# Optimization experiments

Measured on AMD Instinct MI355X. Metric: run time of the kernel, lower is better.

Reference implementation:

```python
import jax, jax.numpy as jnp
import numpy as np

B, N, F = 8, 2048, 256

def setup_inputs() -> dict:
    key = jax.random.key(0)
    ks = jax.random.split(key, 8)
    X = jax.random.normal(ks[0], (B, N, F), dtype=jnp.float32)
    A_geo = jax.random.uniform(ks[1], (N, N), dtype=jnp.float32)
    distance_matrix = jax.random.uniform(ks[2], (N, N), dtype=jnp.float32)
    W_w = jax.random.normal(ks[3], (F, F), dtype=jnp.float32) * 0.05
    W_b = jax.random.normal(ks[4], (F,), dtype=jnp.float32) * 0.05
    a1 = jax.random.normal(ks[5], (F,), dtype=jnp.float32) * 0.05  # attn_fc weight, first half (for h_i)
    a2 = jax.random.normal(ks[6], (F,), dtype=jnp.float32) * 0.05  # attn_fc weight, second half (for h_j)
    attn_b = jax.random.normal(ks[7], (1,), dtype=jnp.float32) * 0.05
    threshold = jnp.ones((1,), dtype=jnp.float32) * 0.3
    return {"X": X, "A_geo": A_geo, "distance_matrix": distance_matrix,
            "W_w": W_w, "W_b": W_b, "a1": a1, "a2": a2,
            "attn_b": attn_b, "threshold": threshold}

def reference(X, A_geo, distance_matrix, W_w, W_b, a1, a2, attn_b, threshold):
    alpha = 0.1  # leaky relu slope
    h = jnp.einsum('bnf,of->bno', X, W_w) + W_b            # (B,N,F)
    # attn_fc(cat(h_i,h_j)) == h_i@a1 + h_j@a2 + b (linear decomposition of concat)
    s1 = jnp.einsum('bnf,f->bn', h, a1)                    # score contribution of h_i
    s2 = jnp.einsum('bnf,f->bn', h, a2)                    # score contribution of h_j
    e = jax.nn.leaky_relu(s1[:, :, None] + s2[:, None, :] + attn_b[0],
                          negative_slope=alpha)            # (B,N,N)
    n = distance_matrix.shape[0]
    idx = jnp.arange(n)
    D = distance_matrix.at[idx, idx].set(1.0)              # fill_diagonal_(1.0)
    e = e + 1.0 / (D + 1e-5)[None, :, :]
    mask = jax.nn.sigmoid(10.0 * (A_geo - threshold[0]))   # (N,N)
    e = e * mask[None, :, :]
    attention = jax.nn.softmax(e, axis=-1)                 # dropout: eval mode (identity)
    h_prime = jnp.einsum('bnm,bmf->bnf', attention, h)
    return h_prime
```

## Files before the change

kernel.cpp:

```cpp
#include <hip/hip_runtime.h>
#include <hip/hip_bf16.h>
#include <math.h>

#define Bsz 8
#define Nn  2048
#define Ff  256
#define KCAP 1024
#define THR 60.0f

typedef short short8 __attribute__((ext_vector_type(8)));
typedef float f32x4  __attribute__((ext_vector_type(4)));
typedef unsigned short u16x4 __attribute__((ext_vector_type(4)));
typedef unsigned short u16x8 __attribute__((ext_vector_type(8)));
typedef unsigned int uint;

static __device__ __forceinline__ unsigned short f2bf(float v) {
    __hip_bfloat16 b = __float2bfloat16(v);
    return *reinterpret_cast<unsigned short*>(&b);
}
static __device__ __forceinline__ float bf2f(unsigned short u) {
    return __uint_as_float((uint)u << 16);
}
static __device__ __forceinline__ float fast_rcp(float x) {
    return __builtin_amdgcn_rcpf(x);
}

__global__ __launch_bounds__(512) void k_h(const float* __restrict__ X,
                                           const float* __restrict__ W,
                                           const float* __restrict__ Wb,
                                           const float* __restrict__ a1,
                                           const float* __restrict__ a2,
                                           unsigned short* __restrict__ h,
                                           float* __restrict__ s1,
                                           float* __restrict__ s2) {
    __shared__ char smem[45056];
    char* w_lds = smem;
    char* x_lds = smem + 32768;
    float (*sred1)[4][16] = (float(*)[4][16])(smem + 40960);
    float (*sred2)[4][16] = (float(*)[4][16])(smem + 40960 + 2048);

    const int tid  = threadIdx.x;
    const int lane = tid & 63;
    const int w    = tid >> 6;
    const int r0   = blockIdx.x * 64;
    const int b    = r0 >> 11;
    const int n0   = r0 & 2047;

    f32x4 acc[2][4];
#pragma unroll
    for (int mt = 0; mt < 2; mt++)
#pragma unroll
        for (int nt = 0; nt < 4; nt++) acc[mt][nt] = (f32x4)0.f;

    float4 wv[8], xv[2];
    auto gload = [&](int kc) {
        const int f0 = kc * 64;
#pragma unroll
        for (int p = 0; p < 8; p++) {
            int idx = tid + p * 512;
            int o = idx >> 4, fi = idx & 15;
            wv[p] = *(const float4*)&W[(size_t)o * Ff + f0 + fi * 4];
        }
#pragma unroll
        for (int p = 0; p < 2; p++) {
            int idx = tid + p * 512;
            int n = idx >> 4, fi = idx & 15;
            xv[p] = *(const float4*)&X[(size_t)(r0 + n) * Ff + f0 + fi * 4];
        }
    };
    auto swrite = [&]() {
#pragma unroll
        for (int p = 0; p < 8; p++) {
            int idx = tid + p * 512;
            int o = idx >> 4, fi = idx & 15;
            u16x4 pk = {f2bf(wv[p].x), f2bf(wv[p].y), f2bf(wv[p].z), f2bf(wv[p].w)};
            *(u16x4*)(w_lds + ((o * 128 + fi * 8) ^ ((o & 7) << 4))) = pk;
        }
#pragma unroll
        for (int p = 0; p < 2; p++) {
            int idx = tid + p * 512;
            int n = idx >> 4, fi = idx & 15;
            u16x4 pk = {f2bf(xv[p].x), f2bf(xv[p].y), f2bf(xv[p].z), f2bf(xv[p].w)};
            *(u16x4*)(x_lds + ((n * 128 + fi * 8) ^ ((n & 7) << 4))) = pk;
        }
    };

    gload(0);
    for (int kc = 0; kc < 4; kc++) {
        __syncthreads();
        swrite();
        __syncthreads();
        if (kc < 3) gload(kc + 1);
#pragma unroll
        for (int kt = 0; kt < 2; kt++) {
            short8 bfr[4];
#pragma unroll
            for (int nt = 0; nt < 4; nt++) {
                int n = nt * 16 + (lane & 15);
                bfr[nt] = *(const short8*)(x_lds + ((n * 128 + kt * 64 + (lane >> 4) * 16) ^ ((n & 7) << 4)));
            }
#pragma unroll
            for (int mt = 0; mt < 2; mt++) {
                int o = w * 32 + mt * 16 + (lane & 15);
                short8 afr = *(const short8*)(w_lds + ((o * 128 + kt * 64 + (lane >> 4) * 16) ^ ((o & 7) << 4)));
#pragma unroll
                for (int nt = 0; nt < 4; nt++)
                    acc[mt][nt] = __builtin_amdgcn_mfma_f32_16x16x32_bf16(afr, bfr[nt], acc[mt][nt], 0, 0, 0);
            }
        }
    }

    __syncthreads();
    float s1p[4] = {0.f, 0.f, 0.f, 0.f};
    float s2p[4] = {0.f, 0.f, 0.f, 0.f};
#pragma unroll
    for (int mt = 0; mt < 2; mt++) {
#pragma unroll
        for (int reg = 0; reg < 4; reg++) {
            int o = w * 32 + mt * 16 + (lane >> 4) * 4 + reg;
            float wb = Wb[o], a1v = a1[o], a2v = a2[o];
#pragma unroll
            for (int nt = 0; nt < 4; nt++) {
                float hv = acc[mt][nt][reg] + wb;
                int nl = nt * 16 + (lane & 15);
                *(unsigned short*)(w_lds + nl * 512 + ((o * 2) ^ ((nl & 7) << 4))) = f2bf(hv);
                s1p[nt] += hv * a1v;
                s2p[nt] += hv * a2v;
            }
        }
    }
#pragma unroll
    for (int nt = 0; nt < 4; nt++) {
        s1p[nt] += __shfl_xor(s1p[nt], 16); s1p[nt] += __shfl_xor(s1p[nt], 32);
        s2p[nt] += __shfl_xor(s2p[nt], 16); s2p[nt] += __shfl_xor(s2p[nt], 32);
    }
    if (lane < 16) {
#pragma unroll
        for (int nt = 0; nt < 4; nt++) { sred1[w][nt][lane] = s1p[nt]; sred2[w][nt][lane] = s2p[nt]; }
    }
    __syncthreads();

#pragma unroll
    for (int p = 0; p < 4; p++) {
        int id = tid + p * 512;
        int nl = id >> 5;
        int c16 = (id & 31) * 16;
        u16x8 v = *(const u16x8*)(w_lds + nl * 512 + (c16 ^ ((nl & 7) << 4)));
        *(u16x8*)&h[((size_t)(b * Nn + n0 + nl)) * Ff + (id & 31) * 8] = v;
    }
    if (tid < 64) {
        int nt = tid >> 4, col = tid & 15;
        float v = 0.f;
#pragma unroll
        for (int k = 0; k < 8; k++) v += sred1[k][nt][col];
        s1[b * Nn + n0 + nt * 16 + col] = v;
    } else if (tid < 128) {
        int t2 = tid - 64;
        int nt = t2 >> 4, col = t2 & 15;
        float v = 0.f;
#pragma unroll
        for (int k = 0; k < 8; k++) v += sred2[k][nt][col];
        s2[b * Nn + n0 + nt * 16 + col] = v;
    }
}

__global__ __launch_bounds__(512) void k_attn(const unsigned short* __restrict__ h,
                                              const float* __restrict__ s1,
                                              const float* __restrict__ s2,
                                              const float* __restrict__ Ageo,
                                              const float* __restrict__ Dm,
                                              const float* __restrict__ ab_p,
                                              const float* __restrict__ thr_p,
                                              float* __restrict__ out) {
    __shared__ uint  ejs[KCAP];
    __shared__ float emks[KCAP];
    __shared__ float edgs[KCAP];
    __shared__ float red[8];
    __shared__ uint  cptr;

    const int i    = blockIdx.x;
    const int tid  = threadIdx.x;
    const int lane = tid & 63;
    const int w    = tid >> 6;
    const float c10 = 10.0f * thr_p[0];

    if (tid == 0) cptr = 0;
    const int j0 = tid * 4;
    float4 a = *(const float4*)&Ageo[(size_t)i * Nn + j0];
    float4 d = *(const float4*)&Dm[(size_t)i * Nn + j0];
    float av[4] = {a.x, a.y, a.z, a.w};
    float dv[4] = {d.x, d.y, d.z, d.w};
    float mk[4], gg[4];
    float m = 0.0f;
#pragma unroll
    for (int c = 0; c < 4; c++) {
        float dd = (j0 + c == i) ? 1.0f : dv[c];
        float mkv = fast_rcp(1.0f + __expf(c10 - 10.0f * av[c]));
        float g   = mkv * fast_rcp(dd + 1e-5f);
        mk[c] = mkv;
        gg[c] = g;
        m = fmaxf(m, g);
    }
#pragma unroll
    for (int dd = 32; dd; dd >>= 1) m = fmaxf(m, __shfl_xor(m, dd));
    if (lane == 0) red[w] = m;
    __syncthreads();
    float gmax = red[0];
#pragma unroll
    for (int k = 1; k < 8; k++) gmax = fmaxf(gmax, red[k]);
    const float cut = gmax - THR;
#pragma unroll
    for (int c = 0; c < 4; c++) {
        if (gg[c] > cut) {
            uint slot = atomicAdd(&cptr, 1u);
            if (slot < KCAP) {
                ejs[slot]  = (uint)(j0 + c);
                emks[slot] = mk[c];
                edgs[slot] = gg[c] - gmax;
            }
        }
    }
    __syncthreads();
    const int C = min(cptr, (uint)KCAP);

    const int b = w;
    const float s1v = s1[b * Nn + i] + ab_p[0];
    const float* s2b = s2 + b * Nn;

    float4 acc = make_float4(0.f, 0.f, 0.f, 0.f);
    float psum = 0.f;

    uint  jA  = ejs[0];
    float mkA = emks[0];
    float dgA = edgs[0];
    float s2A = s2b[jA];
    ushort4 hvA = *(const ushort4*)&h[((size_t)(b * Nn + jA)) * Ff + lane * 4];

    for (int c = 0; c < C; c++) {
        int cn = (c + 1 < C) ? c + 1 : c;
        uint  jB  = ejs[cn];
        float mkB = emks[cn];
        float dgB = edgs[cn];
        float s2B = s2b[jB];
        ushort4 hvB = *(const ushort4*)&h[((size_t)(b * Nn + jB)) * Ff + lane * 4];
        float s = s1v + s2A;
        s = s > 0.f ? s : 0.1f * s;
        float p = __expf(s * mkA + dgA);
        psum += p;
        acc.x += p * bf2f(hvA.x);
        acc.y += p * bf2f(hvA.y);
        acc.z += p * bf2f(hvA.z);
        acc.w += p * bf2f(hvA.w);
        jA = jB; mkA = mkB; dgA = dgB; s2A = s2B; hvA = hvB;
    }

    float inv = 1.0f / psum;
    *(float4*)&out[((size_t)(b * Nn + i)) * Ff + lane * 4] =
        make_float4(acc.x * inv, acc.y * inv, acc.z * inv, acc.w * inv);
}

extern "C" void kernel_launch(void* const* d_in, const int* in_sizes, int n_in,
                              void* d_out, int out_size, void* d_ws, size_t ws_size,
                              hipStream_t stream) {
    const float* X    = (const float*)d_in[0];
    const float* Ageo = (const float*)d_in[1];
    const float* Dm   = (const float*)d_in[2];
    const float* Ww   = (const float*)d_in[3];
    const float* Wb   = (const float*)d_in[4];
    const float* a1   = (const float*)d_in[5];
    const float* a2   = (const float*)d_in[6];
    const float* ab   = (const float*)d_in[7];
    const float* thr  = (const float*)d_in[8];
    float* out = (float*)d_out;

    char* ws = (char*)d_ws;
    float* s1 = (float*)ws;
    float* s2 = s1 + (size_t)Bsz * Nn;
    unsigned short* h = (unsigned short*)(s2 + (size_t)Bsz * Nn);

    k_h<<<256, 512, 0, stream>>>(X, Ww, Wb, a1, a2, h, s1, s2);
    k_attn<<<Nn, 512, 0, stream>>>(h, s1, s2, Ageo, Dm, ab, thr, out);
}
```

Measured before the change: 27.57 us.

## Move edge selection into projection kernel and remap attention blocks per batch

The per-row mask/distance scan and candidate selection move out of the attention kernel into extra blocks of the projection kernel, so they run concurrently with the h GEMM. Selected entries are written to a global list with per-row counters, which a memset zeroes first. The attention kernel now gives each block one batch and 16 rows, so the waves in a block share that batch's h rows instead of spanning all batches. Costs are an extra memset launch, global atomics and a write/read of the entry list, and KCAP drops to 512, which would truncate rows with more candidates.

Result: slower. 37.27 us (+35.2%).

```diff
diff --git a/kernel.cpp b/kernel.cpp
--- a/kernel.cpp
+++ b/kernel.cpp
@@ -5,7 +5,7 @@
 #define Bsz 8
 #define Nn  2048
 #define Ff  256
-#define KCAP 1024
+#define KCAP 512
 #define THR 60.0f
 
 typedef short short8 __attribute__((ext_vector_type(8)));
@@ -25,23 +25,70 @@
     return __builtin_amdgcn_rcpf(x);
 }
 
-__global__ __launch_bounds__(512) void k_h(const float* __restrict__ X,
-                                           const float* __restrict__ W,
-                                           const float* __restrict__ Wb,
-                                           const float* __restrict__ a1,
-                                           const float* __restrict__ a2,
-                                           unsigned short* __restrict__ h,
-                                           float* __restrict__ s1,
-                                           float* __restrict__ s2) {
+__global__ __launch_bounds__(512) void k1(const float* __restrict__ X,
+                                          const float* __restrict__ Ageo,
+                                          const float* __restrict__ Dm,
+                                          const float* __restrict__ W,
+                                          const float* __restrict__ Wb,
+                                          const float* __restrict__ a1,
+                                          const float* __restrict__ a2,
+                                          const float* __restrict__ thr_p,
+                                          unsigned short* __restrict__ h,
+                                          float* __restrict__ s1,
+                                          float* __restrict__ s2,
+                                          uint4* __restrict__ ent,
+                                          uint* __restrict__ cnt) {
     __shared__ char smem[45056];
+    const int tid  = threadIdx.x;
+    const int lane = tid & 63;
+    const int w    = tid >> 6;
+
+    if (blockIdx.x >= 256) {
+        const int i  = blockIdx.x - 256;
+        const int j0 = tid * 4;
+        const float c10 = 10.0f * thr_p[0];
+        float4 a = *(const float4*)&Ageo[(size_t)i * Nn + j0];
+        float4 d = *(const float4*)&Dm[(size_t)i * Nn + j0];
+        float av[4] = {a.x, a.y, a.z, a.w};
+        float dv[4] = {d.x, d.y, d.z, d.w};
+        float mk[4], gg[4];
+        float m = 0.0f;
+#pragma unroll
+        for (int c = 0; c < 4; c++) {
+            float dd = (j0 + c == i) ? 1.0f : dv[c];
+            float mkv = fast_rcp(1.0f + __expf(c10 - 10.0f * av[c]));
+            float g   = mkv * fast_rcp(dd + 1e-5f);
+            mk[c] = mkv;
+            gg[c] = g;
+            m = fmaxf(m, g);
+        }
+#pragma unroll
+        for (int dd = 32; dd; dd >>= 1) m = fmaxf(m, __shfl_xor(m, dd));
+        float* red = (float*)smem;
+        if (lane == 0) red[w] = m;
+        __syncthreads();
+        float gmax = red[0];
+#pragma unroll
+        for (int k = 1; k < 8; k++) gmax = fmaxf(gmax, red[k]);
+        const float cut = gmax - THR;
+#pragma unroll
+        for (int c = 0; c < 4; c++) {
+            if (gg[c] > cut) {
+                uint slot = atomicAdd(&cnt[i], 1u);
+                if (slot < KCAP)
+                    ent[((size_t)i << 9) + slot] =
+                        make_uint4((uint)(j0 + c), __float_as_uint(mk[c]),
+                                   __float_as_uint(gg[c] - gmax), 0u);
+            }
+        }
+        return;
+    }
+
     char* w_lds = smem;
     char* x_lds = smem + 32768;
     float (*sred1)[4][16] = (float(*)[4][16])(smem + 40960);
     float (*sred2)[4][16] = (float(*)[4][16])(smem + 40960 + 2048);
 
-    const int tid  = threadIdx.x;
-    const int lane = tid & 63;
-    const int w    = tid >> 6;
     const int r0   = blockIdx.x * 64;
     const int b    = r0 >> 11;
     const int n0   = r0 & 2047;
@@ -164,99 +211,56 @@
     }
 }
 
-__global__ __launch_bounds__(512) void k_attn(const unsigned short* __restrict__ h,
-                                              const float* __restrict__ s1,
-                                              const float* __restrict__ s2,
-                                              const float* __restrict__ Ageo,
-                                              const float* __restrict__ Dm,
-                                              const float* __restrict__ ab_p,
-                                              const float* __restrict__ thr_p,
-                                              float* __restrict__ out) {
-    __shared__ uint  ejs[KCAP];
-    __shared__ float emks[KCAP];
-    __shared__ float edgs[KCAP];
-    __shared__ float red[8];
-    __shared__ uint  cptr;
-
-    const int i    = blockIdx.x;
-    const int tid  = threadIdx.x;
-    const int lane = tid & 63;
-    const int w    = tid >> 6;
-    const float c10 = 10.0f * thr_p[0];
-
-    if (tid == 0) cptr = 0;
-    const int j0 = tid * 4;
-    float4 a = *(const float4*)&Ageo[(size_t)i * Nn + j0];
-    float4 d = *(const float4*)&Dm[(size_t)i * Nn + j0];
-    float av[4] = {a.x, a.y, a.z, a.w};
-    float dv[4] = {d.x, d.y, d.z, d.w};
-    float mk[4], gg[4];
-    float m = 0.0f;
-#pragma unroll
-    for (int c = 0; c < 4; c++) {
-        float dd = (j0 + c == i) ? 1.0f : dv[c];
-        float mkv = fast_rcp(1.0f + __expf(c10 - 10.0f * av[c]));
-        float g   = mkv * fast_rcp(dd + 1e-5f);
-        mk[c] = mkv;
-        gg[c] = g;
-        m = fmaxf(m, g);
-    }
-#pragma unroll
-    for (int dd = 32; dd; dd >>= 1) m = fmaxf(m, __shfl_xor(m, dd));
-    if (lane == 0) red[w] = m;
-    __syncthreads();
-    float gmax = red[0];
-#pragma unroll
-    for (int k = 1; k < 8; k++) gmax = fmaxf(gmax, red[k]);
-    const float cut = gmax - THR;
-#pragma unroll
-    for (int c = 0; c < 4; c++) {
-        if (gg[c] > cut) {
-            uint slot = atomicAdd(&cptr, 1u);
-            if (slot < KCAP) {
-                ejs[slot]  = (uint)(j0 + c);
-                emks[slot] = mk[c];
-                edgs[slot] = gg[c] - gmax;
-            }
-        }
-    }
-    __syncthreads();
-    const int C = min(cptr, (uint)KCAP);
-
-    const int b = w;
-    const float s1v = s1[b * Nn + i] + ab_p[0];
+__global__ __launch_bounds__(512) void k2(const unsigned short* __restrict__ h,
+                                          const float* __restrict__ s1,
+                                          const float* __restrict__ s2,
+                                          const uint4* __restrict__ ent,
+                                          const uint* __restrict__ cnt,
+                                          const float* __restrict__ ab_p,
+                                          float* __restrict__ out) {
+    const int bid  = blockIdx.x;
+    const int b    = bid & 7;
+    const int i0   = (bid >> 3) * 16;
+    const int lane = threadIdx.x & 63;
+    const int w    = threadIdx.x >> 6;
+    const float ab = ab_p[0];
     const float* s2b = s2 + b * Nn;
-
-    float4 acc = make_float4(0.f, 0.f, 0.f, 0.f);
-    float psum = 0.f;
-
-    uint  jA  = ejs[0];
-    float mkA = emks[0];
-    float dgA = edgs[0];
-    float s2A = s2b[jA];
-    ushort4 hvA = *(const ushort4*)&h[((size_t)(b * Nn + jA)) * Ff + lane * 4];
-
-    for (int c = 0; c < C; c++) {
-        int cn = (c + 1 < C) ? c + 1 : c;
-        uint  jB  = ejs[cn];
-        float mkB = emks[cn];
-        float dgB = edgs[cn];
-        float s2B = s2b[jB];
-        ushort4 hvB = *(const ushort4*)&h[((size_t)(b * Nn + jB)) * Ff + lane * 4];
-        float s = s1v + s2A;
-        s = s > 0.f ? s : 0.1f * s;
-        float p = __expf(s * mkA + dgA);
-        psum += p;
-        acc.x += p * bf2f(hvA.x);
-        acc.y += p * bf2f(hvA.y);
-        acc.z += p * bf2f(hvA.z);
-        acc.w += p * bf2f(hvA.w);
-        jA = jB; mkA = mkB; dgA = dgB; s2A = s2B; hvA = hvB;
-    }
-
-    float inv = 1.0f / psum;
-    *(float4*)&out[((size_t)(b * Nn + i)) * Ff + lane * 4] =
-        make_float4(acc.x * inv, acc.y * inv, acc.z * inv, acc.w * inv);
+    const unsigned short* hb = h + (size_t)b * Nn * Ff;
+
+#pragma unroll
+    for (int rr = 0; rr < 2; rr++) {
+        const int i = i0 + w * 2 + rr;
+        const int C = min(cnt[i], (uint)KCAP);
+        const float s1v = s1[b * Nn + i] + ab;
+        const uint4* el = ent + ((size_t)i << 9);
+
+        float4 acc = make_float4(0.f, 0.f, 0.f, 0.f);
+        float psum = 0.f;
+
+        uint4 e = el[0];
+        float s2A = s2b[e.x];
+        ushort4 hvA = *(const ushort4*)&hb[(size_t)e.x * Ff + lane * 4];
+
+        for (int c = 0; c < C; c++) {
+            int cn = (c + 1 < C) ? c + 1 : c;
+            uint4 en = el[cn];
+            float s2B = s2b[en.x];
+            ushort4 hvB = *(const ushort4*)&hb[(size_t)en.x * Ff + lane * 4];
+            float s = s1v + s2A;
+            s = s > 0.f ? s : 0.1f * s;
+            float p = __expf(s * __uint_as_float(e.y) + __uint_as_float(e.z));
+            psum += p;
+            acc.x += p * bf2f(hvA.x);
+            acc.y += p * bf2f(hvA.y);
+            acc.z += p * bf2f(hvA.z);
+            acc.w += p * bf2f(hvA.w);
+            e = en; s2A = s2B; hvA = hvB;
+        }
+
+        float inv = 1.0f / psum;
+        *(float4*)&out[((size_t)(b * Nn + i)) * Ff + lane * 4] =
+            make_float4(acc.x * inv, acc.y * inv, acc.z * inv, acc.w * inv);
+    }
 }
 
 extern "C" void kernel_launch(void* const* d_in, const int* in_sizes, int n_in,
@@ -274,10 +278,13 @@
     float* out = (float*)d_out;
 
     char* ws = (char*)d_ws;
-    float* s1 = (float*)ws;
-    float* s2 = s1 + (size_t)Bsz * Nn;
+    uint4* ent = (uint4*)ws;
+    uint*  cnt = (uint*)(ws + (size_t)Nn * KCAP * 16);
+    float* s1  = (float*)(cnt + Nn);
+    float* s2  = s1 + (size_t)Bsz * Nn;
     unsigned short* h = (unsigned short*)(s2 + (size_t)Bsz * Nn);
 
-    k_h<<<256, 512, 0, stream>>>(X, Ww, Wb, a1, a2, h, s1, s2);
-    k_attn<<<Nn, 512, 0, stream>>>(h, s1, s2, Ageo, Dm, ab, thr, out);
-}
+    hipMemsetAsync(cnt, 0, Nn * sizeof(uint), stream);
+    k1<<<256 + Nn, 512, 0, stream>>>(X, Ageo, Dm, Ww, Wb, a1, a2, thr, h, s1, s2, ent, cnt);
+    k2<<<1024, 512, 0, stream>>>(h, s1, s2, ent, cnt, ab, out);
+}
```
